# Kernel optimization log

Measured on AMD Instinct MI355X. Metric: run time of the kernel, lower is better.

## Reference

```python
import jax, jax.numpy as jnp
import numpy as np

DIM, R, HEAD = 512, 4, 8
HD = DIM // HEAD
SCALE = HD ** -0.5
EPS = 1e-5


def dwconv(x, w, b, stride, padding):
    # depthwise conv (groups == channels) + bias + relu; x:[B,C,H,W], w:[C,1,kh,kw]
    y = jax.lax.conv_general_dilated(
        x, w, window_strides=stride, padding=padding,
        feature_group_count=x.shape[1],
        dimension_numbers=('NCHW', 'OIHW', 'NCHW'))
    return jax.nn.relu(y + b[None, :, None, None])


def setup_inputs() -> dict:
    key = jax.random.key(0)
    ks = jax.random.split(key, 12)
    s = 0.02
    return {
        'x': jax.random.normal(ks[0], (8, DIM, 56, 56), dtype=jnp.float32),
        'Wq': jax.random.normal(ks[1], (DIM, DIM), dtype=jnp.float32) * s,
        'bq': jnp.zeros((DIM,), jnp.float32),
        'Wkv': jax.random.normal(ks[2], (2 * DIM, DIM), dtype=jnp.float32) * s,
        'bkv': jnp.zeros((2 * DIM,), jnp.float32),
        'w1a': jax.random.normal(ks[3], (DIM, 1, 1, R), dtype=jnp.float32) * s,
        'b1a': jnp.zeros((DIM,), jnp.float32),
        'w1b': jax.random.normal(ks[4], (DIM, 1, R, 1), dtype=jnp.float32) * s,
        'b1b': jnp.zeros((DIM,), jnp.float32),
        'w2': jax.random.normal(ks[5], (DIM, 1, R, R), dtype=jnp.float32) * s,
        'b2': jnp.zeros((DIM,), jnp.float32),
        'w3': jax.random.normal(ks[6], (DIM, 1, 3, 3), dtype=jnp.float32) * s,
        'b3': jnp.zeros((DIM,), jnp.float32),
        'gamma': jnp.ones((DIM,), jnp.float32),
        'beta': jnp.zeros((DIM,), jnp.float32),
    }


def reference(x, Wq, bq, Wkv, bkv, w1a, b1a, w1b, b1b, w2, b2, w3, b3, gamma, beta):
    B, C, H, W = x.shape
    N = H * W
    x_layer = x.reshape(B, C, N).transpose(0, 2, 1)  # [B,N,C]
    q = (x_layer @ Wq.T + bq).reshape(B, N, HEAD, HD).transpose(0, 2, 1, 3)  # [B,h,N,d]

    # branch 1: (1,R)s(1,R) dwconv -> (R,1)s(R,1) dwconv
    l1 = dwconv(dwconv(x, w1a, b1a, (1, R), ((0, 0), (0, 0))),
                w1b, b1b, (R, 1), ((0, 0), (0, 0))).reshape(B, C, -1)
    # branch 2: RxR stride-R dwconv
    l2 = dwconv(x, w2, b2, (R, R), ((0, 0), (0, 0))).reshape(B, C, -1)
    # branch 3: avg-pool to (H/R, W/R) then 3x3 dwconv pad 1
    l3 = x.reshape(B, C, H // R, R, W // R, R).mean(axis=(3, 5))
    l3 = dwconv(l3, w3, b3, (1, 1), ((1, 1), (1, 1))).reshape(B, C, -1)

    l_ = jnp.concatenate([l1, l2, l3], axis=2).transpose(0, 2, 1)  # [B,M,C]
    mu = l_.mean(-1, keepdims=True)
    var = ((l_ - mu) ** 2).mean(-1, keepdims=True)
    l_ = (l_ - mu) * jax.lax.rsqrt(var + EPS) * gamma + beta

    M = l_.shape[1]
    kv = (l_ @ Wkv.T + bkv).reshape(B, M, 2, HEAD, HD).transpose(2, 0, 3, 1, 4)
    k, v = kv[0], kv[1]  # [B,h,M,d]

    attn = jax.nn.softmax(jnp.einsum('bhid,bhjd->bhij', q, k) * SCALE, axis=-1)
    out = jnp.einsum('bhij,bhjd->bhid', attn, v).transpose(0, 2, 1, 3).reshape(B, N, C)
    # NOTE: original torch code computes proj(out) but then overwrites it with
    # proj_drop(out); with drop=0 the returned value is exactly `out`.
    return out
```

## Files before the change

kernel.cpp:

```cpp
#include <hip/hip_runtime.h>
#include <hip/hip_bf16.h>

#define BATCH   8
#define C_DIM   512
#define HWD     56
#define NPIX    3136
#define PW      14
#define PP      196
#define M_TOT   588
#define BM_ROWS 4704
#define BM_PAD  4736
#define HEADS   8
#define HD      64
#define N_SEQ   3136
#define SM_SCALE 0.125f

typedef __attribute__((ext_vector_type(8))) short bf16x8;
typedef __attribute__((ext_vector_type(4))) float f32x4;

__device__ __forceinline__ short f2bs(float f) {
    __hip_bfloat16 h = __float2bfloat16(f);
    return *reinterpret_cast<short*>(&h);
}
__device__ __forceinline__ float bs2f(short s) {
    __hip_bfloat16 h = *reinterpret_cast<__hip_bfloat16*>(&s);
    return __bfloat162float(h);
}

__device__ __forceinline__ void gl_lds16(const void* g, void* l) {
    __builtin_amdgcn_global_load_lds(
        (const __attribute__((address_space(1))) void*)g,
        (__attribute__((address_space(3))) void*)l, 16, 0, 0);
}

__global__ __launch_bounds__(256) void k_branches(
    const float* __restrict__ x,
    const float* __restrict__ w1a, const float* __restrict__ b1a,
    const float* __restrict__ w1b, const float* __restrict__ b1b,
    const float* __restrict__ w2,  const float* __restrict__ b2,
    const float* __restrict__ w3,  const float* __restrict__ b3,
    float* __restrict__ l_pre)
{
    __shared__ float xs[NPIX];
    __shared__ float y1s[HWD * PW];
    __shared__ float pools[PP];
    const int c = blockIdx.x, b = blockIdx.y, tid = threadIdx.x;
    const float* xp = x + ((size_t)(b * C_DIM + c)) * NPIX;
    for (int i = tid; i < NPIX / 4; i += 256)
        ((float4*)xs)[i] = ((const float4*)xp)[i];
    __syncthreads();

    const float wa0 = w1a[c*4+0], wa1 = w1a[c*4+1], wa2 = w1a[c*4+2], wa3 = w1a[c*4+3];
    const float ba = b1a[c];
    for (int i = tid; i < HWD * PW; i += 256) {
        int h = i / PW, w = i % PW;
        const float* r = xs + h * HWD + w * 4;
        float v = ba + r[0]*wa0 + r[1]*wa1 + r[2]*wa2 + r[3]*wa3;
        y1s[i] = fmaxf(v, 0.f);
    }
    if (tid < PP) {
        int h = tid / PW, w = tid % PW;
        float s = 0.f;
        #pragma unroll
        for (int r = 0; r < 4; ++r) {
            const float* rr = xs + (h*4 + r) * HWD + w * 4;
            s += rr[0] + rr[1] + rr[2] + rr[3];
        }
        pools[tid] = s * (1.f / 16.f);
    }
    __syncthreads();

    if (tid < PP) {
        int h = tid / PW, w = tid % PW;
        float* lp = l_pre + ((size_t)(b * C_DIM + c)) * M_TOT;
        float v1 = b1b[c];
        v1 += y1s[(h*4+0)*PW + w] * w1b[c*4+0];
        v1 += y1s[(h*4+1)*PW + w] * w1b[c*4+1];
        v1 += y1s[(h*4+2)*PW + w] * w1b[c*4+2];
        v1 += y1s[(h*4+3)*PW + w] * w1b[c*4+3];
        lp[tid] = fmaxf(v1, 0.f);
        float v2 = b2[c];
        #pragma unroll
        for (int r = 0; r < 4; ++r)
            #pragma unroll
            for (int s2 = 0; s2 < 4; ++s2)
                v2 += xs[(h*4+r)*HWD + w*4 + s2] * w2[c*16 + r*4 + s2];
        lp[PP + tid] = fmaxf(v2, 0.f);
        float v3 = b3[c];
        #pragma unroll
        for (int dh = -1; dh <= 1; ++dh)
            #pragma unroll
            for (int dw = -1; dw <= 1; ++dw) {
                int hh = h + dh, ww = w + dw;
                if (hh >= 0 && hh < PW && ww >= 0 && ww < PW)
                    v3 += pools[hh*PW + ww] * w3[c*9 + (dh+1)*3 + (dw+1)];
            }
        lp[2*PP + tid] = fmaxf(v3, 0.f);
    }
}

__global__ __launch_bounds__(256) void k_stats(
    const float* __restrict__ l_pre, float2* __restrict__ stats)
{
    __shared__ float ssum[4][64];
    __shared__ float ssq[4][64];
    const int tid = threadIdx.x;
    const int ml = tid & 63, cg = tid >> 6;
    const int b = blockIdx.y;
    const int m = blockIdx.x * 64 + ml;
    float s = 0.f, q = 0.f;
    if (m < M_TOT) {
        const float* base = l_pre + ((size_t)b * C_DIM + cg * 128) * M_TOT + m;
        for (int c = 0; c < 128; ++c) {
            float v = base[(size_t)c * M_TOT];
            s += v; q += v * v;
        }
    }
    ssum[cg][ml] = s; ssq[cg][ml] = q;
    __syncthreads();
    if (tid < 64 && blockIdx.x * 64 + tid < M_TOT) {
        float ts = ssum[0][tid] + ssum[1][tid] + ssum[2][tid] + ssum[3][tid];
        float tq = ssq[0][tid] + ssq[1][tid] + ssq[2][tid] + ssq[3][tid];
        float mu = ts * (1.f / 512.f);
        float var = tq * (1.f / 512.f) - mu * mu;
        stats[(size_t)b * M_TOT + blockIdx.x * 64 + tid] =
            make_float2(mu, rsqrtf(var + 1e-5f));
    }
}

__global__ __launch_bounds__(256) void k_wconv(
    const float* __restrict__ Wq, const float* __restrict__ Wkv,
    short* __restrict__ Wqb, short* __restrict__ Wkvb)
{
    int i = (blockIdx.x * 256 + threadIdx.x) * 4;
    if (i < 262144) {
        float4 v = *(const float4*)(Wq + i);
        short o[4] = {f2bs(v.x), f2bs(v.y), f2bs(v.z), f2bs(v.w)};
        *(short4*)(Wqb + i) = *(short4*)o;
    } else {
        int j = i - 262144;
        float4 v = *(const float4*)(Wkv + j);
        short o[4] = {f2bs(v.x), f2bs(v.y), f2bs(v.z), f2bs(v.w)};
        *(short4*)(Wkvb + j) = *(short4*)o;
    }
}

__global__ __launch_bounds__(256) void k_xpose(
    const float* __restrict__ x, short* __restrict__ Xb)
{
    __shared__ float sx[64][68];
    const int tid = threadIdx.x;
    const int n0 = blockIdx.x * 64, c0 = blockIdx.y * 64, b = blockIdx.z;
    #pragma unroll
    for (int it = 0; it < 4; ++it) {
        int idx = tid + it * 256;
        int cr = idx >> 4, n4 = (idx & 15) * 4;
        float4 v = *(const float4*)(x + ((size_t)(b * C_DIM + c0 + cr)) * NPIX + n0 + n4);
        *(float4*)&sx[cr][n4] = v;
    }
    __syncthreads();
    #pragma unroll
    for (int p = 0; p < 2; ++p) {
        int idx = tid + p * 256;
        int nr = idx >> 3, cg = (idx & 7) * 8;
        short ov[8];
        #pragma unroll
        for (int e = 0; e < 8; ++e) ov[e] = f2bs(sx[cg + e][nr]);
        *(float4*)&Xb[((size_t)(b * NPIX + n0 + nr)) * C_DIM + c0 + cg] = *(float4*)ov;
    }
}

__global__ __launch_bounds__(256) void k_lnt(
    const float* __restrict__ l_pre, const float2* __restrict__ stats,
    const float* __restrict__ gamma, const float* __restrict__ beta,
    short* __restrict__ Lb)
{
    __shared__ float sx[64][68];
    const int tid = threadIdx.x;
    const int m0 = blockIdx.x * 64, c0 = blockIdx.y * 64, b = blockIdx.z;
    #pragma unroll
    for (int it = 0; it < 4; ++it) {
        int idx = tid + it * 256;
        int cr = idx >> 4, m4 = (idx & 15) * 4;
        float4 v = {0.f, 0.f, 0.f, 0.f};
        if (m0 + m4 < M_TOT)
            v = *(const float4*)(l_pre + ((size_t)(b * C_DIM + c0 + cr)) * M_TOT + m0 + m4);
        *(float4*)&sx[cr][m4] = v;
    }
    __syncthreads();
    #pragma unroll
    for (int p = 0; p < 2; ++p) {
        int idx = tid + p * 256;
        int mr = idx >> 3, cg = (idx & 7) * 8;
        int m = m0 + mr;
        float mu = 0.f, rstd = 0.f;
        if (m < M_TOT) {
            float2 st = stats[(size_t)b * M_TOT + m];
            mu = st.x; rstd = st.y;
        }
        short ov[8];
        #pragma unroll
        for (int e = 0; e < 8; ++e) {
            int c = c0 + cg + e;
            ov[e] = f2bs((sx[cg + e][mr] - mu) * rstd * gamma[c] + beta[c]);
        }
        if (m < M_TOT)
            *(float4*)&Lb[((size_t)(b * M_TOT + m)) * C_DIM + c0 + cg] = *(float4*)ov;
    }
}

template<int MODE>
__global__ __launch_bounds__(256) void k_gemm(
    const short* __restrict__ A, const short* __restrict__ Bw,
    const float* __restrict__ bias,
    short* __restrict__ Out0, short* __restrict__ Out1)
{
    __shared__ short As[128 * 64];
    __shared__ short Bs[128 * 64];
    const int tid = threadIdx.x;
    const int lane = tid & 63, w = tid >> 6;
    const int l15 = lane & 15, quad = lane >> 4;
    const int wr = w & 1, wc = w >> 1;
    const int row0 = blockIdx.x * 128, col0 = blockIdx.y * 128;
    const int lr8 = lane >> 3, lc8 = (lane & 7) * 8;

    f32x4 acc[4][4] = {};

    for (int c0 = 0; c0 < 512; c0 += 64) {
        __syncthreads();
        #pragma unroll
        for (int it = 0; it < 4; ++it) {
            int r = w * 32 + it * 8;
            gl_lds16(A  + (size_t)(row0 + r + lr8) * 512 + c0 + lc8, &As[r * 64]);
            gl_lds16(Bw + (size_t)(col0 + r + lr8) * 512 + c0 + lc8, &Bs[r * 64]);
        }
        __syncthreads();
        #pragma unroll
        for (int ks = 0; ks < 2; ++ks) {
            bf16x8 af[4], bf[4];
            #pragma unroll
            for (int t = 0; t < 4; ++t) {
                af[t] = *(const bf16x8*)&As[(wr*64 + t*16 + l15)*64 + ks*32 + quad*8];
                bf[t] = *(const bf16x8*)&Bs[(wc*64 + t*16 + l15)*64 + ks*32 + quad*8];
            }
            #pragma unroll
            for (int nt = 0; nt < 4; ++nt)
                #pragma unroll
                for (int mt = 0; mt < 4; ++mt)
                    acc[nt][mt] = __builtin_amdgcn_mfma_f32_16x16x32_bf16(
                        af[nt], bf[mt], acc[nt][mt], 0, 0, 0);
        }
    }

    #pragma unroll
    for (int nt = 0; nt < 4; ++nt) {
        int row_t = row0 + wr * 64 + nt * 16 + quad * 4;
        #pragma unroll
        for (int mt = 0; mt < 4; ++mt) {
            int col = col0 + wc * 64 + mt * 16 + l15;
            float bv = bias[col];
            #pragma unroll
            for (int r = 0; r < 4; ++r) {
                int row_g = row_t + r;
                float v = acc[nt][mt][r] + bv;
                if (MODE == 0) {
                    int b = row_g / N_SEQ;
                    int n = row_g - b * N_SEQ;
                    int h = col >> 6, d = col & 63;
                    Out0[(((size_t)(b * HEADS + h)) * N_SEQ + n) * HD + d] = f2bs(v);
                } else {
                    if (row_g < BM_ROWS) {
                        int b = row_g / M_TOT;
                        int m = row_g - b * M_TOT;
                        if (col < 512) {
                            int h = col >> 6, d = col & 63;
                            Out0[(((size_t)(b * HEADS + h)) * M_TOT + m) * HD + d] = f2bs(v);
                        } else {
                            int jj = col - 512, h = jj >> 6, d = jj & 63;
                            Out1[(((size_t)(b * HEADS + h)) * HD + d) * M_TOT + m] = f2bs(v);
                        }
                    }
                }
            }
        }
    }
}

__global__ __launch_bounds__(256) void k_attn(
    const short* __restrict__ Qb, const short* __restrict__ Kb,
    const short* __restrict__ Vt, float* __restrict__ out)
{
    __shared__ __align__(16) short Qs[64][72];
    __shared__ __align__(16) short Ks[64][72];
    __shared__ __align__(16) short Vs[64][72];
    __shared__ __align__(16) short Ps[64][72];
    const int tid = threadIdx.x;
    const int lane = tid & 63, w = tid >> 6;
    const int l15 = lane & 15, quad = lane >> 4;
    const int n0 = blockIdx.x * 64, h = blockIdx.y, b = blockIdx.z;
    const size_t bh = (size_t)(b * HEADS + h);
    const size_t qbase = (bh * N_SEQ + n0) * HD;
    const size_t kbase = bh * M_TOT * HD;
    const size_t vbase = bh * (size_t)HD * M_TOT;

    #pragma unroll
    for (int it = 0; it < 2; ++it) {
        int idx = tid + it * 256;
        int row = idx >> 3, seg = idx & 7;
        *(float4*)&Qs[row][seg * 8] =
            *(const float4*)(Qb + qbase + (size_t)row * HD + seg * 8);
    }

    f32x4 oacc[4] = {};
    float rs[4] = {0.f, 0.f, 0.f, 0.f};

    __syncthreads();
    bf16x8 qf[2];
    #pragma unroll
    for (int ks = 0; ks < 2; ++ks)
        qf[ks] = *(const bf16x8*)&Qs[w * 16 + l15][ks * 32 + quad * 8];

    for (int jc0 = 0; jc0 < M_TOT; jc0 += 64) {
        if (jc0 + 64 <= M_TOT) {
            #pragma unroll
            for (int it = 0; it < 2; ++it) {
                int idx = tid + it * 256;
                int row = idx >> 3, seg = idx & 7;
                *(float4*)&Ks[row][seg * 8] =
                    *(const float4*)(Kb + kbase + (size_t)(jc0 + row) * HD + seg * 8);
                *(float4*)&Vs[row][seg * 8] =
                    *(const float4*)(Vt + vbase + (size_t)row * M_TOT + jc0 + seg * 8);
            }
        } else {
            #pragma unroll
            for (int it = 0; it < 2; ++it) {
                int idx = tid + it * 256;
                int row = idx >> 3, seg = idx & 7;
                int jg = jc0 + row;
                if (jg < M_TOT) {
                    *(float4*)&Ks[row][seg * 8] =
                        *(const float4*)(Kb + kbase + (size_t)jg * HD + seg * 8);
                } else {
                    float4 z = {0.f, 0.f, 0.f, 0.f};
                    *(float4*)&Ks[row][seg * 8] = z;
                }
                #pragma unroll
                for (int t2 = 0; t2 < 8; ++t2) {
                    int jj = jc0 + seg * 8 + t2;
                    Vs[row][seg * 8 + t2] = (jj < M_TOT)
                        ? Vt[vbase + (size_t)row * M_TOT + jj] : (short)0;
                }
            }
        }
        __syncthreads();

        f32x4 sacc[4] = {};
        #pragma unroll
        for (int nt = 0; nt < 4; ++nt)
            #pragma unroll
            for (int ks = 0; ks < 2; ++ks) {
                bf16x8 kf = *(const bf16x8*)&Ks[nt * 16 + l15][ks * 32 + quad * 8];
                sacc[nt] = __builtin_amdgcn_mfma_f32_16x16x32_bf16(
                    qf[ks], kf, sacc[nt], 0, 0, 0);
            }

        float psum[4] = {0.f, 0.f, 0.f, 0.f};
        #pragma unroll
        for (int nt = 0; nt < 4; ++nt) {
            int jg = jc0 + nt * 16 + l15;
            #pragma unroll
            for (int r = 0; r < 4; ++r) {
                float p = (jg < M_TOT) ? __expf(sacc[nt][r] * SM_SCALE) : 0.f;
                short pb = f2bs(p);
                Ps[w * 16 + quad * 4 + r][nt * 16 + l15] = pb;
                psum[r] += bs2f(pb);
            }
        }
        #pragma unroll
        for (int r = 0; r < 4; ++r) {
            float v = psum[r];
            v += __shfl_xor(v, 1); v += __shfl_xor(v, 2);
            v += __shfl_xor(v, 4); v += __shfl_xor(v, 8);
            rs[r] += v;
        }

        bf16x8 pf[2];
        #pragma unroll
        for (int ks = 0; ks < 2; ++ks)
            pf[ks] = *(const bf16x8*)&Ps[w * 16 + l15][ks * 32 + quad * 8];
        #pragma unroll
        for (int dt = 0; dt < 4; ++dt)
            #pragma unroll
            for (int ks = 0; ks < 2; ++ks) {
                bf16x8 vf = *(const bf16x8*)&Vs[dt * 16 + l15][ks * 32 + quad * 8];
                oacc[dt] = __builtin_amdgcn_mfma_f32_16x16x32_bf16(
                    pf[ks], vf, oacc[dt], 0, 0, 0);
            }
        __syncthreads();
    }

    #pragma unroll
    for (int r = 0; r < 4; ++r) {
        float inv = 1.f / rs[r];
        int n = n0 + w * 16 + quad * 4 + r;
        #pragma unroll
        for (int dt = 0; dt < 4; ++dt)
            out[((size_t)b * N_SEQ + n) * C_DIM + h * HD + dt * 16 + l15] =
                oacc[dt][r] * inv;
    }
}

extern "C" void kernel_launch(void* const* d_in, const int* in_sizes, int n_in,
                              void* d_out, int out_size, void* d_ws, size_t ws_size,
                              hipStream_t stream) {
    const float* x     = (const float*)d_in[0];
    const float* Wq    = (const float*)d_in[1];
    const float* bq    = (const float*)d_in[2];
    const float* Wkv   = (const float*)d_in[3];
    const float* bkv   = (const float*)d_in[4];
    const float* w1a   = (const float*)d_in[5];
    const float* b1a   = (const float*)d_in[6];
    const float* w1b   = (const float*)d_in[7];
    const float* b1b   = (const float*)d_in[8];
    const float* w2    = (const float*)d_in[9];
    const float* b2    = (const float*)d_in[10];
    const float* w3    = (const float*)d_in[11];
    const float* b3    = (const float*)d_in[12];
    const float* gamma = (const float*)d_in[13];
    const float* beta  = (const float*)d_in[14];
    float* out = (float*)d_out;

    char* ws = (char*)d_ws;
    short*  Xb    = (short*)ws;
    float*  l_pre = (float*)ws;
    float2* stats = (float2*)(ws + 9633792);
    short*  Lb    = (short*)(ws + 9671424);
    short*  Wqb   = (short*)(ws + 25690112);
    short*  Wkvb  = (short*)(ws + 26214400);
    short*  Kb    = (short*)(ws + 27262976);
    short*  Vt    = (short*)(ws + 32079872);
    short*  Qb    = (short*)(ws + 36896768);

    k_wconv<<<768, 256, 0, stream>>>(Wq, Wkv, Wqb, Wkvb);
    k_xpose<<<dim3(49, 8, BATCH), 256, 0, stream>>>(x, Xb);
    k_gemm<0><<<dim3(196, 4), 256, 0, stream>>>(Xb, Wqb, bq, Qb, nullptr);
    k_branches<<<dim3(C_DIM, BATCH), 256, 0, stream>>>(
        x, w1a, b1a, w1b, b1b, w2, b2, w3, b3, l_pre);
    k_stats<<<dim3(10, BATCH), 256, 0, stream>>>(l_pre, stats);
    k_lnt<<<dim3(10, 8, BATCH), 256, 0, stream>>>(l_pre, stats, gamma, beta, Lb);
    k_gemm<1><<<dim3(37, 8), 256, 0, stream>>>(Lb, Wkvb, bkv, Kb, Vt);
    k_attn<<<dim3(49, HEADS, BATCH), 256, 0, stream>>>(Qb, Kb, Vt, out);
}
```

Baseline: 293.3 us.

## Keep attention probabilities in registers via transposed MFMA and lane shuffles

The attention kernel now computes S^T (K as A operand, Q as B) so each lane holds probabilities for one query row. It packs them to bf16 and rearranges them into the PV MFMA operand with cross-lane shuffles, which removes the Ps shared-memory round trip and one barrier-dependent LDS read/write per tile. The row sum becomes a single scalar per lane, reduced once at the end instead of per tile. Output is staged through LDS (reusing K/V space) so global stores are float4 coalesced rows. The GEMM template is also split into two plain kernels, which is mostly a refactor. The shuffle permutation is intricate and could introduce correctness risk.

```diff
diff --git a/kernel.cpp b/kernel.cpp
--- a/kernel.cpp
+++ b/kernel.cpp
@@ -22,9 +22,9 @@
     __hip_bfloat16 h = __float2bfloat16(f);
     return *reinterpret_cast<short*>(&h);
 }
-__device__ __forceinline__ float bs2f(short s) {
-    __hip_bfloat16 h = *reinterpret_cast<__hip_bfloat16*>(&s);
-    return __bfloat162float(h);
+__device__ __forceinline__ unsigned pkbf(float lo, float hi) {
+    __hip_bfloat162 t = __float22bfloat162_rn(make_float2(lo, hi));
+    return *reinterpret_cast<unsigned*>(&t);
 }
 
 __device__ __forceinline__ void gl_lds16(const void* g, void* l) {
@@ -209,11 +209,9 @@
     }
 }
 
-template<int MODE>
-__global__ __launch_bounds__(256) void k_gemm(
+__global__ __launch_bounds__(256) void k_gemm_q(
     const short* __restrict__ A, const short* __restrict__ Bw,
-    const float* __restrict__ bias,
-    short* __restrict__ Out0, short* __restrict__ Out1)
+    const float* __restrict__ bias, short* __restrict__ Qb)
 {
     __shared__ short As[128 * 64];
     __shared__ short Bs[128 * 64];
@@ -259,26 +257,81 @@
         for (int mt = 0; mt < 4; ++mt) {
             int col = col0 + wc * 64 + mt * 16 + l15;
             float bv = bias[col];
+            int h = col >> 6, d = col & 63;
+            #pragma unroll
+            for (int r = 0; r < 4; ++r) {
+                int row_g = row_t + r;
+                int b = row_g / N_SEQ;
+                int n = row_g - b * N_SEQ;
+                Qb[(((size_t)(b * HEADS + h)) * N_SEQ + n) * HD + d] =
+                    f2bs(acc[nt][mt][r] + bv);
+            }
+        }
+    }
+}
+
+__global__ __launch_bounds__(256) void k_gemm_kv(
+    const short* __restrict__ A, const short* __restrict__ Bw,
+    const float* __restrict__ bias,
+    short* __restrict__ Kb, short* __restrict__ Vt)
+{
+    __shared__ short As[128 * 64];
+    __shared__ short Bs[128 * 64];
+    const int tid = threadIdx.x;
+    const int lane = tid & 63, w = tid >> 6;
+    const int l15 = lane & 15, quad = lane >> 4;
+    const int wr = w & 1, wc = w >> 1;
+    const int row0 = blockIdx.x * 128, col0 = blockIdx.y * 128;
+    const int lr8 = lane >> 3, lc8 = (lane & 7) * 8;
+
+    f32x4 acc[4][4] = {};
+
+    for (int c0 = 0; c0 < 512; c0 += 64) {
+        __syncthreads();
+        #pragma unroll
+        for (int it = 0; it < 4; ++it) {
+            int r = w * 32 + it * 8;
+            gl_lds16(A  + (size_t)(row0 + r + lr8) * 512 + c0 + lc8, &As[r * 64]);
+            gl_lds16(Bw + (size_t)(col0 + r + lr8) * 512 + c0 + lc8, &Bs[r * 64]);
+        }
+        __syncthreads();
+        #pragma unroll
+        for (int ks = 0; ks < 2; ++ks) {
+            bf16x8 af[4], bf[4];
+            #pragma unroll
+            for (int t = 0; t < 4; ++t) {
+                af[t] = *(const bf16x8*)&As[(wr*64 + t*16 + l15)*64 + ks*32 + quad*8];
+                bf[t] = *(const bf16x8*)&Bs[(wc*64 + t*16 + l15)*64 + ks*32 + quad*8];
+            }
+            #pragma unroll
+            for (int nt = 0; nt < 4; ++nt)
+                #pragma unroll
+                for (int mt = 0; mt < 4; ++mt)
+                    acc[nt][mt] = __builtin_amdgcn_mfma_f32_16x16x32_bf16(
+                        af[nt], bf[mt], acc[nt][mt], 0, 0, 0);
+        }
+    }
+
+    #pragma unroll
+    for (int nt = 0; nt < 4; ++nt) {
+        int row_t = row0 + wr * 64 + nt * 16 + quad * 4;
+        #pragma unroll
+        for (int mt = 0; mt < 4; ++mt) {
+            int col = col0 + wc * 64 + mt * 16 + l15;
+            float bv = bias[col];
             #pragma unroll
             for (int r = 0; r < 4; ++r) {
                 int row_g = row_t + r;
                 float v = acc[nt][mt][r] + bv;
-                if (MODE == 0) {
-                    int b = row_g / N_SEQ;
-                    int n = row_g - b * N_SEQ;
-                    int h = col >> 6, d = col & 63;
-                    Out0[(((size_t)(b * HEADS + h)) * N_SEQ + n) * HD + d] = f2bs(v);
-                } else {
-                    if (row_g < BM_ROWS) {
-                        int b = row_g / M_TOT;
-                        int m = row_g - b * M_TOT;
-                        if (col < 512) {
-                            int h = col >> 6, d = col & 63;
-                            Out0[(((size_t)(b * HEADS + h)) * M_TOT + m) * HD + d] = f2bs(v);
-                        } else {
-                            int jj = col - 512, h = jj >> 6, d = jj & 63;
-                            Out1[(((size_t)(b * HEADS + h)) * HD + d) * M_TOT + m] = f2bs(v);
-                        }
+                if (row_g < BM_ROWS) {
+                    int b = row_g / M_TOT;
+                    int m = row_g - b * M_TOT;
+                    if (col < 512) {
+                        int h = col >> 6, d = col & 63;
+                        Kb[(((size_t)(b * HEADS + h)) * M_TOT + m) * HD + d] = f2bs(v);
+                    } else {
+                        int jj = col - 512, h = jj >> 6, d = jj & 63;
+                        Vt[(((size_t)(b * HEADS + h)) * HD + d) * M_TOT + m] = f2bs(v);
                     }
                 }
             }
@@ -290,10 +343,12 @@
     const short* __restrict__ Qb, const short* __restrict__ Kb,
     const short* __restrict__ Vt, float* __restrict__ out)
 {
-    __shared__ __align__(16) short Qs[64][72];
-    __shared__ __align__(16) short Ks[64][72];
-    __shared__ __align__(16) short Vs[64][72];
-    __shared__ __align__(16) short Ps[64][72];
+    __shared__ __align__(16) short smem[3 * 64 * 72];
+    short* Qs = smem;
+    short* Ks = smem + 64 * 72;
+    short* Vs = smem + 2 * 64 * 72;
+    float* Os = (float*)(smem + 64 * 72);
+
     const int tid = threadIdx.x;
     const int lane = tid & 63, w = tid >> 6;
     const int l15 = lane & 15, quad = lane >> 4;
@@ -307,18 +362,18 @@
     for (int it = 0; it < 2; ++it) {
         int idx = tid + it * 256;
         int row = idx >> 3, seg = idx & 7;
-        *(float4*)&Qs[row][seg * 8] =
+        *(float4*)&Qs[row * 72 + seg * 8] =
             *(const float4*)(Qb + qbase + (size_t)row * HD + seg * 8);
     }
 
     f32x4 oacc[4] = {};
-    float rs[4] = {0.f, 0.f, 0.f, 0.f};
+    float rs = 0.f;
 
     __syncthreads();
     bf16x8 qf[2];
     #pragma unroll
     for (int ks = 0; ks < 2; ++ks)
-        qf[ks] = *(const bf16x8*)&Qs[w * 16 + l15][ks * 32 + quad * 8];
+        qf[ks] = *(const bf16x8*)&Qs[(w * 16 + l15) * 72 + ks * 32 + quad * 8];
 
     for (int jc0 = 0; jc0 < M_TOT; jc0 += 64) {
         if (jc0 + 64 <= M_TOT) {
@@ -326,9 +381,9 @@
             for (int it = 0; it < 2; ++it) {
                 int idx = tid + it * 256;
                 int row = idx >> 3, seg = idx & 7;
-                *(float4*)&Ks[row][seg * 8] =
+                *(float4*)&Ks[row * 72 + seg * 8] =
                     *(const float4*)(Kb + kbase + (size_t)(jc0 + row) * HD + seg * 8);
-                *(float4*)&Vs[row][seg * 8] =
+                *(float4*)&Vs[row * 72 + seg * 8] =
                     *(const float4*)(Vt + vbase + (size_t)row * M_TOT + jc0 + seg * 8);
             }
         } else {
@@ -338,16 +393,16 @@
                 int row = idx >> 3, seg = idx & 7;
                 int jg = jc0 + row;
                 if (jg < M_TOT) {
-                    *(float4*)&Ks[row][seg * 8] =
+                    *(float4*)&Ks[row * 72 + seg * 8] =
                         *(const float4*)(Kb + kbase + (size_t)jg * HD + seg * 8);
                 } else {
                     float4 z = {0.f, 0.f, 0.f, 0.f};
-                    *(float4*)&Ks[row][seg * 8] = z;
+                    *(float4*)&Ks[row * 72 + seg * 8] = z;
                 }
                 #pragma unroll
                 for (int t2 = 0; t2 < 8; ++t2) {
                     int jj = jc0 + seg * 8 + t2;
-                    Vs[row][seg * 8 + t2] = (jj < M_TOT)
+                    Vs[row * 72 + seg * 8 + t2] = (jj < M_TOT)
                         ? Vt[vbase + (size_t)row * M_TOT + jj] : (short)0;
                 }
             }
@@ -356,57 +411,85 @@
 
         f32x4 sacc[4] = {};
         #pragma unroll
-        for (int nt = 0; nt < 4; ++nt)
+        for (int t = 0; t < 4; ++t)
             #pragma unroll
             for (int ks = 0; ks < 2; ++ks) {
-                bf16x8 kf = *(const bf16x8*)&Ks[nt * 16 + l15][ks * 32 + quad * 8];
-                sacc[nt] = __builtin_amdgcn_mfma_f32_16x16x32_bf16(
-                    qf[ks], kf, sacc[nt], 0, 0, 0);
-            }
-
-        float psum[4] = {0.f, 0.f, 0.f, 0.f};
-        #pragma unroll
-        for (int nt = 0; nt < 4; ++nt) {
-            int jg = jc0 + nt * 16 + l15;
-            #pragma unroll
-            for (int r = 0; r < 4; ++r) {
-                float p = (jg < M_TOT) ? __expf(sacc[nt][r] * SM_SCALE) : 0.f;
-                short pb = f2bs(p);
-                Ps[w * 16 + quad * 4 + r][nt * 16 + l15] = pb;
-                psum[r] += bs2f(pb);
-            }
-        }
-        #pragma unroll
-        for (int r = 0; r < 4; ++r) {
-            float v = psum[r];
-            v += __shfl_xor(v, 1); v += __shfl_xor(v, 2);
-            v += __shfl_xor(v, 4); v += __shfl_xor(v, 8);
-            rs[r] += v;
-        }
-
-        bf16x8 pf[2];
-        #pragma unroll
-        for (int ks = 0; ks < 2; ++ks)
-            pf[ks] = *(const bf16x8*)&Ps[w * 16 + l15][ks * 32 + quad * 8];
-        #pragma unroll
-        for (int dt = 0; dt < 4; ++dt)
-            #pragma unroll
-            for (int ks = 0; ks < 2; ++ks) {
-                bf16x8 vf = *(const bf16x8*)&Vs[dt * 16 + l15][ks * 32 + quad * 8];
+                bf16x8 kf = *(const bf16x8*)&Ks[(t * 16 + l15) * 72 + ks * 32 + quad * 8];
+                sacc[t] = __builtin_amdgcn_mfma_f32_16x16x32_bf16(
+                    kf, qf[ks], sacc[t], 0, 0, 0);
+            }
+
+        float p[4][4];
+        if (jc0 + 64 <= M_TOT) {
+            #pragma unroll
+            for (int t = 0; t < 4; ++t)
+                #pragma unroll
+                for (int r = 0; r < 4; ++r) {
+                    p[t][r] = __expf(sacc[t][r] * SM_SCALE);
+                    rs += p[t][r];
+                }
+        } else {
+            #pragma unroll
+            for (int t = 0; t < 4; ++t)
+                #pragma unroll
+                for (int r = 0; r < 4; ++r) {
+                    int jg = jc0 + t * 16 + quad * 4 + r;
+                    float pv = (jg < M_TOT) ? __expf(sacc[t][r] * SM_SCALE) : 0.f;
+                    p[t][r] = pv;
+                    rs += pv;
+                }
+        }
+        unsigned pk[4][2];
+        #pragma unroll
+        for (int t = 0; t < 4; ++t) {
+            pk[t][0] = pkbf(p[t][0], p[t][1]);
+            pk[t][1] = pkbf(p[t][2], p[t][3]);
+        }
+
+        const bool c0 = (quad & 1) != 0, c1 = (quad & 2) != 0;
+        #pragma unroll
+        for (int kc = 0; kc < 2; ++kc) {
+            const int ta = 2 * kc, tb = 2 * kc + 1;
+            unsigned P0x = pk[ta][0], P0y = pk[ta][1];
+            unsigned P1x = pk[tb][0], P1y = pk[tb][1];
+            unsigned X0x = __shfl_xor(P0x, 16), X0y = __shfl_xor(P0y, 16);
+            unsigned X1x = __shfl_xor(P1x, 16), X1y = __shfl_xor(P1y, 16);
+            unsigned Y0x = __shfl_xor(P0x, 32), Y0y = __shfl_xor(P0y, 32);
+            unsigned Y1x = __shfl_xor(P1x, 32), Y1y = __shfl_xor(P1y, 32);
+            unsigned Z0x = __shfl_xor(X0x, 32), Z0y = __shfl_xor(X0y, 32);
+            unsigned Z1x = __shfl_xor(X1x, 32), Z1y = __shfl_xor(X1y, 32);
+            unsigned pv4[4];
+            pv4[0] = c1 ? (c0 ? X1x : Y1x) : (c0 ? Z0x : P0x);
+            pv4[1] = c1 ? (c0 ? X1y : Y1y) : (c0 ? Z0y : P0y);
+            pv4[2] = c1 ? (c0 ? P1x : Z1x) : (c0 ? Y0x : X0x);
+            pv4[3] = c1 ? (c0 ? P1y : Z1y) : (c0 ? Y0y : X0y);
+            bf16x8 pf;
+            __builtin_memcpy(&pf, pv4, 16);
+            #pragma unroll
+            for (int dt = 0; dt < 4; ++dt) {
+                bf16x8 vf = *(const bf16x8*)&Vs[(dt * 16 + l15) * 72 + kc * 32 + quad * 8];
                 oacc[dt] = __builtin_amdgcn_mfma_f32_16x16x32_bf16(
-                    pf[ks], vf, oacc[dt], 0, 0, 0);
-            }
+                    vf, pf, oacc[dt], 0, 0, 0);
+            }
+        }
         __syncthreads();
     }
 
-    #pragma unroll
-    for (int r = 0; r < 4; ++r) {
-        float inv = 1.f / rs[r];
-        int n = n0 + w * 16 + quad * 4 + r;
-        #pragma unroll
-        for (int dt = 0; dt < 4; ++dt)
-            out[((size_t)b * N_SEQ + n) * C_DIM + h * HD + dt * 16 + l15] =
-                oacc[dt][r] * inv;
+    rs += __shfl_xor(rs, 16);
+    rs += __shfl_xor(rs, 32);
+    float inv = 1.f / rs;
+    #pragma unroll
+    for (int dt = 0; dt < 4; ++dt)
+        #pragma unroll
+        for (int r = 0; r < 4; ++r)
+            Os[(w * 16 + l15) * 68 + dt * 16 + quad * 4 + r] = oacc[dt][r] * inv;
+    __syncthreads();
+    #pragma unroll
+    for (int it = 0; it < 4; ++it) {
+        int row = (tid >> 4) + it * 16;
+        int c4 = (tid & 15) * 4;
+        float4 v = *(const float4*)&Os[row * 68 + c4];
+        *(float4*)&out[((size_t)b * N_SEQ + n0 + row) * C_DIM + h * HD + c4] = v;
     }
 }
 
@@ -443,11 +526,11 @@
 
     k_wconv<<<768, 256, 0, stream>>>(Wq, Wkv, Wqb, Wkvb);
     k_xpose<<<dim3(49, 8, BATCH), 256, 0, stream>>>(x, Xb);
-    k_gemm<0><<<dim3(196, 4), 256, 0, stream>>>(Xb, Wqb, bq, Qb, nullptr);
+    k_gemm_q<<<dim3(196, 4), 256, 0, stream>>>(Xb, Wqb, bq, Qb);
     k_branches<<<dim3(C_DIM, BATCH), 256, 0, stream>>>(
         x, w1a, b1a, w1b, b1b, w2, b2, w3, b3, l_pre);
     k_stats<<<dim3(10, BATCH), 256, 0, stream>>>(l_pre, stats);
     k_lnt<<<dim3(10, 8, BATCH), 256, 0, stream>>>(l_pre, stats, gamma, beta, Lb);
-    k_gemm<1><<<dim3(37, 8), 256, 0, stream>>>(Lb, Wkvb, bkv, Kb, Vt);
+    k_gemm_kv<<<dim3(37, 8), 256, 0, stream>>>(Lb, Wkvb, bkv, Kb, Vt);
     k_attn<<<dim3(49, HEADS, BATCH), 256, 0, stream>>>(Qb, Kb, Vt, out);
 }
```

Result: slower. 309.0 us (+5.4%).
